# Optimization experiments

Measured on AMD Instinct MI355X. Metric: run time of the kernel, lower is better.

Reference implementation:

```python
import jax, jax.numpy as jnp
import numpy as np

N, E, F, H = 50000, 1_600_000, 6, 64


def setup_inputs() -> dict:
    key = jax.random.key(0)
    ks = jax.random.split(key, 12)
    inp = {
        "vertex_features": jax.random.normal(ks[0], (N, F), dtype=jnp.float32),
        "edges": jax.random.randint(ks[1], (2, E), 0, N, dtype=jnp.int64 if jax.config.jax_enable_x64 else jnp.int32),
        "weights": jax.random.uniform(ks[2], (E,), dtype=jnp.float32),
        # GCNConv layer params (glorot-ish scale) + biases (PyG default bias=True)
        "W1": jax.random.normal(ks[3], (F, H), dtype=jnp.float32) / np.sqrt(F),
        "b1": jnp.zeros((H,), jnp.float32),
        "W2": jax.random.normal(ks[4], (H, H), dtype=jnp.float32) / np.sqrt(H),
        "b2": jnp.zeros((H,), jnp.float32),
        "W3": jax.random.normal(ks[5], (H, H), dtype=jnp.float32) / np.sqrt(H),
        "b3": jnp.zeros((H,), jnp.float32),
        "Wl": jax.random.normal(ks[6], (H, 1), dtype=jnp.float32) / np.sqrt(H),
        "bl": jnp.zeros((1,), jnp.float32),
    }
    return inp


def _gcn_norm(edges, weights, n):
    # PyG gcn_norm: add self loops (weight 1), symmetric D^-1/2 A D^-1/2;
    # degree computed at target nodes (edge_index[1], flow source_to_target).
    row, col = edges[0], edges[1]
    loop = jnp.arange(n, dtype=row.dtype)
    row_f = jnp.concatenate([row, loop])
    col_f = jnp.concatenate([col, loop])
    w_f = jnp.concatenate([weights, jnp.ones((n,), weights.dtype)])
    deg = jax.ops.segment_sum(w_f, col_f, num_segments=n)
    dis = jnp.where(deg > 0, jax.lax.rsqrt(jnp.maximum(deg, 1e-30)), 0.0)
    norm = dis[row_f] * w_f * dis[col_f]
    return row_f, col_f, norm


def _gcn_conv(x, W, b, row, col, norm, n):
    xw = x @ W                                   # [n, H_out]
    agg = jax.ops.segment_sum(norm[:, None] * xw[row], col, num_segments=n)
    return agg + b


def reference(vertex_features, edges, weights, W1, b1, W2, b2, W3, b3, Wl, bl):
    n = vertex_features.shape[0]
    row, col, norm = _gcn_norm(edges, weights, n)  # norm identical for all layers
    h = jax.nn.sigmoid(_gcn_conv(vertex_features, W1, b1, row, col, norm, n))
    h = jax.nn.sigmoid(_gcn_conv(h, W2, b2, row, col, norm, n))
    h = jax.nn.sigmoid(_gcn_conv(h, W3, b3, row, col, norm, n))
    logits = h @ Wl + bl                           # [n, 1]
    return jax.nn.softmax(logits, axis=0)          # softmax over node dim
```

## Files before the change

### kernel.cpp

```cpp
#include <hip/hip_runtime.h>
#include <math.h>


#define BLK 256
#define SKB 256
#define CHUNK 4096

typedef __attribute__((ext_vector_type(8))) short bf16x8;
typedef __attribute__((ext_vector_type(4))) float f32x4;

__device__ inline unsigned short f2bf(float f) {
  unsigned u = __float_as_uint(f);
  return (unsigned short)((u + 0x7FFF + ((u >> 16) & 1)) >> 16);
}
__device__ inline float bflo(unsigned u) { return __uint_as_float(u << 16); }
__device__ inline float bfhi(unsigned u) { return __uint_as_float(u & 0xFFFF0000u); }


__global__ __launch_bounds__(256) void k_binscatter(
    const int* __restrict__ row, const int* __restrict__ col,
    const float* __restrict__ w, int E,
    int* __restrict__ bfill, int2* __restrict__ bucket, int CAP) {
  __shared__ int2 stage[CHUNK];
  __shared__ int lhist[SKB], lbase[SKB], gbase[SKB], lfill[SKB];
  int t = threadIdx.x;
  int e0 = blockIdx.x * CHUNK;
  int n = E - e0; if (n > CHUNK) n = CHUNK;
  lhist[t] = 0; lfill[t] = 0;
  __syncthreads();
  for (int i = t; i < n; i += BLK) atomicAdd(&lhist[((unsigned)col[e0 + i]) >> 8], 1);
  __syncthreads();
  lbase[t] = lhist[t];
  __syncthreads();
  for (int off = 1; off < SKB; off <<= 1) {
    int v = (t >= off) ? lbase[t - off] : 0;
    __syncthreads();
    lbase[t] += v;
    __syncthreads();
  }
  int excl = lbase[t] - lhist[t];
  int cb = lhist[t];
  gbase[t] = cb ? atomicAdd(&bfill[t << 4], cb) : 0;
  __syncthreads();
  lbase[t] = excl;
  __syncthreads();
  for (int i = t; i < n; i += BLK) {
    int c = col[e0 + i];
    int b = ((unsigned)c) >> 8;
    int r = atomicAdd(&lfill[b], 1);
    stage[lbase[b] + r] = make_int2(row[e0 + i] | (c << 16), __float_as_int(w[e0 + i]));
  }
  __syncthreads();
  for (int i = t; i < n; i += BLK) {
    int2 p = stage[i];
    int b = ((unsigned)p.x) >> 24;
    bucket[(size_t)b * CAP + gbase[b] + (i - lbase[b])] = p;
  }
}


__global__ __launch_bounds__(256) void k_build(
    const int2* __restrict__ bucket, const int* __restrict__ bfill,
    const float* __restrict__ x,
    unsigned* __restrict__ csr, int* __restrict__ cnt, int* __restrict__ start,
    float* __restrict__ dis, unsigned short* __restrict__ x8b, int CAP, int N) {
  __shared__ int   hist[SKB];
  __shared__ float wsum[SKB];
  __shared__ int   lstart[SKB + 1];
  __shared__ int   lfill[SKB];
  int b = blockIdx.x, t = threadIdx.x;
  int n0 = b << 8;
  int M = N - n0; if (M > 256) M = 256;
  if (M <= 0) return;
  hist[t] = 0; wsum[t] = 0.0f; lfill[t] = 0;
  __syncthreads();
  const int2* bb = bucket + (size_t)b * CAP;
  int ec = bfill[b << 4];
  for (int i = t; i < ec; i += BLK) {
    int2 p = bb[i];
    int lc = (((unsigned)p.x) >> 16) & 255;
    atomicAdd(&hist[lc], 1);
    atomicAdd(&wsum[lc], __int_as_float(p.y));
  }
  __syncthreads();
  if (t == 0) {
    int run = 0;
    for (int i = 0; i < M; ++i) { lstart[i] = run; run += hist[i]; }
    lstart[M] = run;
  }
  __syncthreads();
  if (t < M) {
    int n = n0 + t;
    cnt[n] = hist[t];
    start[n] = b * CAP + lstart[t];
    float d = 1.0f / sqrtf(wsum[t] + 1.0f);
    dis[n] = d;
    const float* xr = x + (size_t)n * 6;
    uint4 pk;
    pk.x = (unsigned)f2bf(d * xr[0]) | ((unsigned)f2bf(d * xr[1]) << 16);
    pk.y = (unsigned)f2bf(d * xr[2]) | ((unsigned)f2bf(d * xr[3]) << 16);
    pk.z = (unsigned)f2bf(d * xr[4]) | ((unsigned)f2bf(d * xr[5]) << 16);
    pk.w = 0u;
    *(uint4*)(x8b + (size_t)n * 8) = pk;
  }
  __syncthreads();
  for (int i = t; i < ec; i += BLK) {
    int2 p = bb[i];
    int lc = (((unsigned)p.x) >> 16) & 255;
    int pos = lstart[lc] + atomicAdd(&lfill[lc], 1);
    csr[(size_t)b * CAP + pos] =
        ((unsigned)p.x & 0xFFFFu) | ((unsigned)f2bf(__int_as_float(p.y)) << 16);
  }
}


__global__ void k_wprep(const float* __restrict__ W2, const float* __restrict__ W3,
                        unsigned short* __restrict__ W2b, unsigned short* __restrict__ W3b) {
  int i = blockIdx.x * blockDim.x + threadIdx.x;
  if (i < 4096) { W2b[i] = f2bf(W2[i]); W3b[i] = f2bf(W3[i]); }
}


__global__ void k_layer1(const unsigned short* __restrict__ x8b,
                         const int* __restrict__ start, const int* __restrict__ cnt,
                         const unsigned* __restrict__ csr, const float* __restrict__ dis,
                         const float* __restrict__ W1, const float* __restrict__ b1,
                         unsigned short* __restrict__ hb, int N) {
  int n = blockIdx.x * blockDim.x + threadIdx.x;
  if (n >= N) return;
  uint4 sv = *(const uint4*)(x8b + (size_t)n * 8);
  float a0 = bflo(sv.x), a1 = bfhi(sv.x), a2 = bflo(sv.y);
  float a3 = bfhi(sv.y), a4 = bflo(sv.z), a5 = bfhi(sv.z);
  int s = start[n], e = s + cnt[n];
  int i = s;
  for (; i + 4 <= e; i += 4) {
    unsigned p0 = csr[i], p1 = csr[i + 1], p2 = csr[i + 2], p3 = csr[i + 3];
    uint4 h0 = *(const uint4*)(x8b + (size_t)(p0 & 0xFFFFu) * 8);
    uint4 h1 = *(const uint4*)(x8b + (size_t)(p1 & 0xFFFFu) * 8);
    uint4 h2 = *(const uint4*)(x8b + (size_t)(p2 & 0xFFFFu) * 8);
    uint4 h3 = *(const uint4*)(x8b + (size_t)(p3 & 0xFFFFu) * 8);
    float v0 = bfhi(p0), v1 = bfhi(p1), v2 = bfhi(p2), v3 = bfhi(p3);
    a0 += v0*bflo(h0.x) + v1*bflo(h1.x) + v2*bflo(h2.x) + v3*bflo(h3.x);
    a1 += v0*bfhi(h0.x) + v1*bfhi(h1.x) + v2*bfhi(h2.x) + v3*bfhi(h3.x);
    a2 += v0*bflo(h0.y) + v1*bflo(h1.y) + v2*bflo(h2.y) + v3*bflo(h3.y);
    a3 += v0*bfhi(h0.y) + v1*bfhi(h1.y) + v2*bfhi(h2.y) + v3*bfhi(h3.y);
    a4 += v0*bflo(h0.z) + v1*bflo(h1.z) + v2*bflo(h2.z) + v3*bflo(h3.z);
    a5 += v0*bfhi(h0.z) + v1*bfhi(h1.z) + v2*bfhi(h2.z) + v3*bfhi(h3.z);
  }
  for (; i < e; ++i) {
    unsigned pe = csr[i];
    float v = bfhi(pe);
    uint4 hv = *(const uint4*)(x8b + (size_t)(pe & 0xFFFFu) * 8);
    a0 += v * bflo(hv.x); a1 += v * bfhi(hv.x);
    a2 += v * bflo(hv.y); a3 += v * bfhi(hv.y);
    a4 += v * bflo(hv.z); a5 += v * bfhi(hv.z);
  }
  float d = dis[n];
  a0 *= d; a1 *= d; a2 *= d; a3 *= d; a4 *= d; a5 *= d;
  unsigned short* o = hb + (size_t)n * 64;
#pragma unroll
  for (int j4 = 0; j4 < 16; ++j4) {
    float4 acc = *(const float4*)(b1 + j4 * 4);
    const float* Wc = W1 + j4 * 4;
    acc.x += a0*Wc[0] + a1*Wc[64] + a2*Wc[128] + a3*Wc[192] + a4*Wc[256] + a5*Wc[320];
    acc.y += a0*Wc[1] + a1*Wc[65] + a2*Wc[129] + a3*Wc[193] + a4*Wc[257] + a5*Wc[321];
    acc.z += a0*Wc[2] + a1*Wc[66] + a2*Wc[130] + a3*Wc[194] + a4*Wc[258] + a5*Wc[322];
    acc.w += a0*Wc[3] + a1*Wc[67] + a2*Wc[131] + a3*Wc[195] + a4*Wc[259] + a5*Wc[323];
    uint2 pk;
    pk.x = (unsigned)f2bf(d / (1.0f + expf(-acc.x))) |
           ((unsigned)f2bf(d / (1.0f + expf(-acc.y))) << 16);
    pk.y = (unsigned)f2bf(d / (1.0f + expf(-acc.z))) |
           ((unsigned)f2bf(d / (1.0f + expf(-acc.w))) << 16);
    *(uint2*)(o + j4 * 4) = pk;
  }
}


__global__ void k_agg64(const unsigned short* __restrict__ hb,
                        const int* __restrict__ start, const int* __restrict__ cnt,
                        const unsigned* __restrict__ csr, const float* __restrict__ dis,
                        unsigned short* __restrict__ aggb, int N) {
  int t = blockIdx.x * blockDim.x + threadIdx.x;
  int n = t >> 3, sub = t & 7;
  if (n >= N) return;
  uint4 sv = *(const uint4*)(hb + (size_t)n * 64 + sub * 8);
  float a0 = bflo(sv.x), a1 = bfhi(sv.x), a2 = bflo(sv.y), a3 = bfhi(sv.y);
  float a4 = bflo(sv.z), a5 = bfhi(sv.z), a6 = bflo(sv.w), a7 = bfhi(sv.w);
  int s = start[n], e = s + cnt[n];
  int i = s;
  for (; i + 4 <= e; i += 4) {
    unsigned p0 = csr[i], p1 = csr[i + 1], p2 = csr[i + 2], p3 = csr[i + 3];
    uint4 h0 = *(const uint4*)(hb + (size_t)(p0 & 0xFFFFu) * 64 + sub * 8);
    uint4 h1 = *(const uint4*)(hb + (size_t)(p1 & 0xFFFFu) * 64 + sub * 8);
    uint4 h2 = *(const uint4*)(hb + (size_t)(p2 & 0xFFFFu) * 64 + sub * 8);
    uint4 h3 = *(const uint4*)(hb + (size_t)(p3 & 0xFFFFu) * 64 + sub * 8);
    float v0 = bfhi(p0), v1 = bfhi(p1), v2 = bfhi(p2), v3 = bfhi(p3);
    a0 += v0*bflo(h0.x) + v1*bflo(h1.x) + v2*bflo(h2.x) + v3*bflo(h3.x);
    a1 += v0*bfhi(h0.x) + v1*bfhi(h1.x) + v2*bfhi(h2.x) + v3*bfhi(h3.x);
    a2 += v0*bflo(h0.y) + v1*bflo(h1.y) + v2*bflo(h2.y) + v3*bflo(h3.y);
    a3 += v0*bfhi(h0.y) + v1*bfhi(h1.y) + v2*bfhi(h2.y) + v3*bfhi(h3.y);
    a4 += v0*bflo(h0.z) + v1*bflo(h1.z) + v2*bflo(h2.z) + v3*bflo(h3.z);
    a5 += v0*bfhi(h0.z) + v1*bfhi(h1.z) + v2*bfhi(h2.z) + v3*bfhi(h3.z);
    a6 += v0*bflo(h0.w) + v1*bflo(h1.w) + v2*bflo(h2.w) + v3*bflo(h3.w);
    a7 += v0*bfhi(h0.w) + v1*bfhi(h1.w) + v2*bfhi(h2.w) + v3*bfhi(h3.w);
  }
  for (; i < e; ++i) {
    unsigned pe = csr[i];
    float v = bfhi(pe);
    uint4 hv = *(const uint4*)(hb + (size_t)(pe & 0xFFFFu) * 64 + sub * 8);
    a0 += v * bflo(hv.x); a1 += v * bfhi(hv.x);
    a2 += v * bflo(hv.y); a3 += v * bfhi(hv.y);
    a4 += v * bflo(hv.z); a5 += v * bfhi(hv.z);
    a6 += v * bflo(hv.w); a7 += v * bfhi(hv.w);
  }
  float d = dis[n];
  uint4 pk;
  pk.x = (unsigned)f2bf(d * a0) | ((unsigned)f2bf(d * a1) << 16);
  pk.y = (unsigned)f2bf(d * a2) | ((unsigned)f2bf(d * a3) << 16);
  pk.z = (unsigned)f2bf(d * a4) | ((unsigned)f2bf(d * a5) << 16);
  pk.w = (unsigned)f2bf(d * a6) | ((unsigned)f2bf(d * a7) << 16);
  *(uint4*)(aggb + (size_t)n * 64 + sub * 8) = pk;
}


__global__ __launch_bounds__(256) void k_dense64_mfma(
    const unsigned short* __restrict__ aggb, const unsigned short* __restrict__ Wb,
    const float* __restrict__ b, const float* __restrict__ dis,
    unsigned short* __restrict__ hb, int NS) {
  int wid = threadIdx.x >> 6, lane = threadIdx.x & 63;
  int quad = lane >> 4, r16 = lane & 15;
  bf16x8 Bf[2][4];
#pragma unroll
  for (int kt = 0; kt < 2; ++kt)
#pragma unroll
    for (int jt = 0; jt < 4; ++jt)
#pragma unroll
      for (int j = 0; j < 8; ++j)
        Bf[kt][jt][j] = (short)Wb[(kt * 32 + quad * 8 + j) * 64 + jt * 16 + r16];
  float bias[4];
#pragma unroll
  for (int jt = 0; jt < 4; ++jt) bias[jt] = b[jt * 16 + r16];
  int stride = gridDim.x * 4;
  for (int s = blockIdx.x * 4 + wid; s < NS; s += stride) {
    int n0 = s * 16;
    bf16x8 Af0 = *(const bf16x8*)(aggb + (size_t)(n0 + r16) * 64 + quad * 8);
    bf16x8 Af1 = *(const bf16x8*)(aggb + (size_t)(n0 + r16) * 64 + 32 + quad * 8);
    f32x4 C[4];
#pragma unroll
    for (int jt = 0; jt < 4; ++jt) {
      f32x4 z = {0.f, 0.f, 0.f, 0.f};
      z = __builtin_amdgcn_mfma_f32_16x16x32_bf16(Af0, Bf[0][jt], z, 0, 0, 0);
      z = __builtin_amdgcn_mfma_f32_16x16x32_bf16(Af1, Bf[1][jt], z, 0, 0, 0);
      C[jt] = z;
    }
    float dv[4];
#pragma unroll
    for (int reg = 0; reg < 4; ++reg) dv[reg] = dis[n0 + quad * 4 + reg];
#pragma unroll
    for (int jt = 0; jt < 4; ++jt)
#pragma unroll
      for (int reg = 0; reg < 4; ++reg) {
        float h = dv[reg] / (1.0f + expf(-(C[jt][reg] + bias[jt])));
        hb[(size_t)(n0 + quad * 4 + reg) * 64 + jt * 16 + r16] = f2bf(h);
      }
  }
}


__global__ __launch_bounds__(256) void k_head_mfma(
    const unsigned short* __restrict__ aggb, const unsigned short* __restrict__ Wb,
    const float* __restrict__ b, const float* __restrict__ Wl,
    const float* __restrict__ bl, float* __restrict__ expv,
    float* __restrict__ red_part, int NS) {
  int wid = threadIdx.x >> 6, lane = threadIdx.x & 63;
  int quad = lane >> 4, r16 = lane & 15;
  bf16x8 Bf[2][4];
#pragma unroll
  for (int kt = 0; kt < 2; ++kt)
#pragma unroll
    for (int jt = 0; jt < 4; ++jt)
#pragma unroll
      for (int j = 0; j < 8; ++j)
        Bf[kt][jt][j] = (short)Wb[(kt * 32 + quad * 8 + j) * 64 + jt * 16 + r16];
  float bias[4], wlv[4];
#pragma unroll
  for (int jt = 0; jt < 4; ++jt) {
    bias[jt] = b[jt * 16 + r16];
    wlv[jt]  = Wl[jt * 16 + r16];
  }
  float bl0 = bl[0];
  float lsum = 0.0f;
  int stride = gridDim.x * 4;
  for (int s = blockIdx.x * 4 + wid; s < NS; s += stride) {
    int n0 = s * 16;
    bf16x8 Af0 = *(const bf16x8*)(aggb + (size_t)(n0 + r16) * 64 + quad * 8);
    bf16x8 Af1 = *(const bf16x8*)(aggb + (size_t)(n0 + r16) * 64 + 32 + quad * 8);
    f32x4 C[4];
#pragma unroll
    for (int jt = 0; jt < 4; ++jt) {
      f32x4 z = {0.f, 0.f, 0.f, 0.f};
      z = __builtin_amdgcn_mfma_f32_16x16x32_bf16(Af0, Bf[0][jt], z, 0, 0, 0);
      z = __builtin_amdgcn_mfma_f32_16x16x32_bf16(Af1, Bf[1][jt], z, 0, 0, 0);
      C[jt] = z;
    }
    float p0 = 0, p1 = 0, p2 = 0, p3 = 0;
#pragma unroll
    for (int jt = 0; jt < 4; ++jt) {
      p0 += wlv[jt] / (1.0f + expf(-(C[jt][0] + bias[jt])));
      p1 += wlv[jt] / (1.0f + expf(-(C[jt][1] + bias[jt])));
      p2 += wlv[jt] / (1.0f + expf(-(C[jt][2] + bias[jt])));
      p3 += wlv[jt] / (1.0f + expf(-(C[jt][3] + bias[jt])));
    }
#pragma unroll
    for (int m = 1; m < 16; m <<= 1) {
      p0 += __shfl_xor(p0, m, 64);
      p1 += __shfl_xor(p1, m, 64);
      p2 += __shfl_xor(p2, m, 64);
      p3 += __shfl_xor(p3, m, 64);
    }
    float ls = 0.0f;
    if (r16 == 0) {
      float e0 = expf(p0 + bl0), e1 = expf(p1 + bl0);
      float e2 = expf(p2 + bl0), e3 = expf(p3 + bl0);
      int r = n0 + quad * 4;
      expv[r] = e0; expv[r + 1] = e1; expv[r + 2] = e2; expv[r + 3] = e3;
      ls = e0 + e1 + e2 + e3;
    }
    ls += __shfl_xor(ls, 16, 64);
    ls += __shfl_xor(ls, 32, 64);
    lsum += ls;
  }
  if (lane == 0) atomicAdd(&red_part[(blockIdx.x & 63) << 4], lsum);
}

__global__ void k_out(const float* __restrict__ expv, int N,
                      const float* __restrict__ red_part, float* __restrict__ out) {
  int i = blockIdx.x * blockDim.x + threadIdx.x;
  int lane = threadIdx.x & 63;
  float s = red_part[lane << 4];
#pragma unroll
  for (int o = 32; o > 0; o >>= 1) s += __shfl_down(s, o, 64);
  s = __shfl(s, 0, 64);
  if (i < N) out[i] = expv[i] / s;
}


extern "C" void kernel_launch(void* const* d_in, const int* in_sizes, int n_in,
                              void* d_out, int out_size, void* d_ws, size_t ws_size,
                              hipStream_t stream) {
  const float* x   = (const float*)d_in[0];
  const int*   edg = (const int*)d_in[1];
  const float* w   = (const float*)d_in[2];
  const float* W1  = (const float*)d_in[3];
  const float* b1  = (const float*)d_in[4];
  const float* W2  = (const float*)d_in[5];
  const float* b2  = (const float*)d_in[6];
  const float* W3  = (const float*)d_in[7];
  const float* b3  = (const float*)d_in[8];
  const float* Wl  = (const float*)d_in[9];
  const float* bl  = (const float*)d_in[10];
  float* out = (float*)d_out;

  const int N = in_sizes[0] / 6;
  const int E = in_sizes[2];
  const int* row = edg;
  const int* col = edg + E;
  const int NB = (N + 255) >> 8;
  const int NS = (N + 15) / 16;

  size_t off = 0;
  char* base = (char*)d_ws;
  auto alloc = [&](size_t bytes) -> void* {
    void* p = base + off;
    off += (bytes + 255) & ~(size_t)255;
    return p;
  };
  int*   bfill    = (int*)alloc((size_t)SKB * 16 * 4);
  float* red_part = (float*)alloc((size_t)64 * 16 * 4);
  size_t zero_bytes = off;
  int*   cnt    = (int*)alloc((size_t)N * 4);
  int*   start  = (int*)alloc((size_t)N * 4);
  float* dis    = (float*)alloc((size_t)N * 4);
  float* expv   = (float*)alloc((size_t)N * 4);
  unsigned short* x8b = (unsigned short*)alloc((size_t)N * 8 * 2);
  unsigned short* hb  = (unsigned short*)alloc((size_t)N * 64 * 2);
  unsigned short* W2b = (unsigned short*)alloc(4096 * 2);
  unsigned short* W3b = (unsigned short*)alloc(4096 * 2);
  size_t remain = (ws_size > off) ? (ws_size - off) : 0;
  long long capn = ((long long)remain) / ((long long)NB * 12);
  int CAP = (int)capn;
  if (CAP > 9216) CAP = 9216;
  if (CAP < 8704) CAP = 8704;
  unsigned* csr = (unsigned*)alloc((size_t)NB * CAP * 4);
  size_t aggsz = (size_t)N * 64 * 2;
  size_t bksz  = (size_t)NB * CAP * 8;
  void* shared_blk = alloc(aggsz > bksz ? aggsz : bksz);
  int2*           bucket = (int2*)shared_blk;
  unsigned short* aggb   = (unsigned short*)shared_blk;

  const int gE  = (E + CHUNK - 1) / CHUNK;
  const int gN  = (N + BLK - 1) / BLK;
  const int gN8 = (N * 8 + BLK - 1) / BLK;
  const int gM  = 200;

  hipMemsetAsync(d_ws, 0, zero_bytes, stream);

  k_wprep     <<<16, BLK, 0, stream>>>(W2, W3, W2b, W3b);
  k_binscatter<<<gE, BLK, 0, stream>>>(row, col, w, E, bfill, bucket, CAP);
  k_build     <<<NB, BLK, 0, stream>>>(bucket, bfill, x, csr, cnt, start, dis, x8b, CAP, N);

  k_layer1<<<gN, BLK, 0, stream>>>(x8b, start, cnt, csr, dis, W1, b1, hb, N);

  k_agg64       <<<gN8, BLK, 0, stream>>>(hb, start, cnt, csr, dis, aggb, N);
  k_dense64_mfma<<<gM,  BLK, 0, stream>>>(aggb, W2b, b2, dis, hb, NS);

  k_agg64    <<<gN8, BLK, 0, stream>>>(hb, start, cnt, csr, dis, aggb, N);
  k_head_mfma<<<gM,  BLK, 0, stream>>>(aggb, W3b, b3, Wl, bl, expv, red_part, NS);

  k_out<<<gN, BLK, 0, stream>>>(expv, N, red_part, out);
}
```

Measured before the change: 232.4 us.

## Unroll gathers by eight, widen build blocks, fold weight prep into build

The CSR gather loops in layer1 and agg64 go from 4-way to 8-way unrolled, so more independent neighbor loads are in flight per thread. k_build now runs with 512 threads per block and gains 8 extra blocks that do the bf16 conversion of W2/W3, which removes the separate k_wprep launch. The binscatter CHUNK is halved, giving more, smaller scatter blocks. The wider unroll raises register pressure, and the mix of unrelated tweaks can pull in different directions.

```diff
diff --git a/kernel.cpp b/kernel.cpp
--- a/kernel.cpp
+++ b/kernel.cpp
@@ -3,8 +3,9 @@
 
 
 #define BLK 256
+#define BLKB 512
 #define SKB 256
-#define CHUNK 4096
+#define CHUNK 2048
 
 typedef __attribute__((ext_vector_type(8))) short bf16x8;
 typedef __attribute__((ext_vector_type(4))) float f32x4;
@@ -59,24 +60,31 @@
 }
 
 
-__global__ __launch_bounds__(256) void k_build(
+__global__ __launch_bounds__(512) void k_build(
     const int2* __restrict__ bucket, const int* __restrict__ bfill,
     const float* __restrict__ x,
     unsigned* __restrict__ csr, int* __restrict__ cnt, int* __restrict__ start,
-    float* __restrict__ dis, unsigned short* __restrict__ x8b, int CAP, int N) {
+    float* __restrict__ dis, unsigned short* __restrict__ x8b, int CAP, int N,
+    int NBb, const float* __restrict__ W2, const float* __restrict__ W3,
+    unsigned short* __restrict__ W2b, unsigned short* __restrict__ W3b) {
   __shared__ int   hist[SKB];
   __shared__ float wsum[SKB];
   __shared__ int   lstart[SKB + 1];
   __shared__ int   lfill[SKB];
   int b = blockIdx.x, t = threadIdx.x;
+  if (b >= NBb) {
+    int i = (b - NBb) * BLKB + t;
+    if (i < 4096) { W2b[i] = f2bf(W2[i]); W3b[i] = f2bf(W3[i]); }
+    return;
+  }
   int n0 = b << 8;
   int M = N - n0; if (M > 256) M = 256;
   if (M <= 0) return;
-  hist[t] = 0; wsum[t] = 0.0f; lfill[t] = 0;
+  if (t < SKB) { hist[t] = 0; wsum[t] = 0.0f; lfill[t] = 0; }
   __syncthreads();
   const int2* bb = bucket + (size_t)b * CAP;
   int ec = bfill[b << 4];
-  for (int i = t; i < ec; i += BLK) {
+  for (int i = t; i < ec; i += BLKB) {
     int2 p = bb[i];
     int lc = (((unsigned)p.x) >> 16) & 255;
     atomicAdd(&hist[lc], 1);
@@ -104,20 +112,13 @@
     *(uint4*)(x8b + (size_t)n * 8) = pk;
   }
   __syncthreads();
-  for (int i = t; i < ec; i += BLK) {
+  for (int i = t; i < ec; i += BLKB) {
     int2 p = bb[i];
     int lc = (((unsigned)p.x) >> 16) & 255;
     int pos = lstart[lc] + atomicAdd(&lfill[lc], 1);
     csr[(size_t)b * CAP + pos] =
         ((unsigned)p.x & 0xFFFFu) | ((unsigned)f2bf(__int_as_float(p.y)) << 16);
   }
-}
-
-
-__global__ void k_wprep(const float* __restrict__ W2, const float* __restrict__ W3,
-                        unsigned short* __restrict__ W2b, unsigned short* __restrict__ W3b) {
-  int i = blockIdx.x * blockDim.x + threadIdx.x;
-  if (i < 4096) { W2b[i] = f2bf(W2[i]); W3b[i] = f2bf(W3[i]); }
 }
 
 
@@ -133,19 +134,31 @@
   float a3 = bfhi(sv.y), a4 = bflo(sv.z), a5 = bfhi(sv.z);
   int s = start[n], e = s + cnt[n];
   int i = s;
-  for (; i + 4 <= e; i += 4) {
-    unsigned p0 = csr[i], p1 = csr[i + 1], p2 = csr[i + 2], p3 = csr[i + 3];
+  for (; i + 8 <= e; i += 8) {
+    unsigned p0 = csr[i],     p1 = csr[i + 1], p2 = csr[i + 2], p3 = csr[i + 3];
+    unsigned p4 = csr[i + 4], p5 = csr[i + 5], p6 = csr[i + 6], p7 = csr[i + 7];
     uint4 h0 = *(const uint4*)(x8b + (size_t)(p0 & 0xFFFFu) * 8);
     uint4 h1 = *(const uint4*)(x8b + (size_t)(p1 & 0xFFFFu) * 8);
     uint4 h2 = *(const uint4*)(x8b + (size_t)(p2 & 0xFFFFu) * 8);
     uint4 h3 = *(const uint4*)(x8b + (size_t)(p3 & 0xFFFFu) * 8);
+    uint4 h4 = *(const uint4*)(x8b + (size_t)(p4 & 0xFFFFu) * 8);
+    uint4 h5 = *(const uint4*)(x8b + (size_t)(p5 & 0xFFFFu) * 8);
+    uint4 h6 = *(const uint4*)(x8b + (size_t)(p6 & 0xFFFFu) * 8);
+    uint4 h7 = *(const uint4*)(x8b + (size_t)(p7 & 0xFFFFu) * 8);
     float v0 = bfhi(p0), v1 = bfhi(p1), v2 = bfhi(p2), v3 = bfhi(p3);
-    a0 += v0*bflo(h0.x) + v1*bflo(h1.x) + v2*bflo(h2.x) + v3*bflo(h3.x);
-    a1 += v0*bfhi(h0.x) + v1*bfhi(h1.x) + v2*bfhi(h2.x) + v3*bfhi(h3.x);
-    a2 += v0*bflo(h0.y) + v1*bflo(h1.y) + v2*bflo(h2.y) + v3*bflo(h3.y);
-    a3 += v0*bfhi(h0.y) + v1*bfhi(h1.y) + v2*bfhi(h2.y) + v3*bfhi(h3.y);
-    a4 += v0*bflo(h0.z) + v1*bflo(h1.z) + v2*bflo(h2.z) + v3*bflo(h3.z);
-    a5 += v0*bfhi(h0.z) + v1*bfhi(h1.z) + v2*bfhi(h2.z) + v3*bfhi(h3.z);
+    float v4 = bfhi(p4), v5 = bfhi(p5), v6 = bfhi(p6), v7 = bfhi(p7);
+    a0 += v0*bflo(h0.x) + v1*bflo(h1.x) + v2*bflo(h2.x) + v3*bflo(h3.x)
+        + v4*bflo(h4.x) + v5*bflo(h5.x) + v6*bflo(h6.x) + v7*bflo(h7.x);
+    a1 += v0*bfhi(h0.x) + v1*bfhi(h1.x) + v2*bfhi(h2.x) + v3*bfhi(h3.x)
+        + v4*bfhi(h4.x) + v5*bfhi(h5.x) + v6*bfhi(h6.x) + v7*bfhi(h7.x);
+    a2 += v0*bflo(h0.y) + v1*bflo(h1.y) + v2*bflo(h2.y) + v3*bflo(h3.y)
+        + v4*bflo(h4.y) + v5*bflo(h5.y) + v6*bflo(h6.y) + v7*bflo(h7.y);
+    a3 += v0*bfhi(h0.y) + v1*bfhi(h1.y) + v2*bfhi(h2.y) + v3*bfhi(h3.y)
+        + v4*bfhi(h4.y) + v5*bfhi(h5.y) + v6*bfhi(h6.y) + v7*bfhi(h7.y);
+    a4 += v0*bflo(h0.z) + v1*bflo(h1.z) + v2*bflo(h2.z) + v3*bflo(h3.z)
+        + v4*bflo(h4.z) + v5*bflo(h5.z) + v6*bflo(h6.z) + v7*bflo(h7.z);
+    a5 += v0*bfhi(h0.z) + v1*bfhi(h1.z) + v2*bfhi(h2.z) + v3*bfhi(h3.z)
+        + v4*bfhi(h4.z) + v5*bfhi(h5.z) + v6*bfhi(h6.z) + v7*bfhi(h7.z);
   }
   for (; i < e; ++i) {
     unsigned pe = csr[i];
@@ -188,21 +201,35 @@
   float a4 = bflo(sv.z), a5 = bfhi(sv.z), a6 = bflo(sv.w), a7 = bfhi(sv.w);
   int s = start[n], e = s + cnt[n];
   int i = s;
-  for (; i + 4 <= e; i += 4) {
-    unsigned p0 = csr[i], p1 = csr[i + 1], p2 = csr[i + 2], p3 = csr[i + 3];
+  for (; i + 8 <= e; i += 8) {
+    unsigned p0 = csr[i],     p1 = csr[i + 1], p2 = csr[i + 2], p3 = csr[i + 3];
+    unsigned p4 = csr[i + 4], p5 = csr[i + 5], p6 = csr[i + 6], p7 = csr[i + 7];
     uint4 h0 = *(const uint4*)(hb + (size_t)(p0 & 0xFFFFu) * 64 + sub * 8);
     uint4 h1 = *(const uint4*)(hb + (size_t)(p1 & 0xFFFFu) * 64 + sub * 8);
     uint4 h2 = *(const uint4*)(hb + (size_t)(p2 & 0xFFFFu) * 64 + sub * 8);
     uint4 h3 = *(const uint4*)(hb + (size_t)(p3 & 0xFFFFu) * 64 + sub * 8);
+    uint4 h4 = *(const uint4*)(hb + (size_t)(p4 & 0xFFFFu) * 64 + sub * 8);
+    uint4 h5 = *(const uint4*)(hb + (size_t)(p5 & 0xFFFFu) * 64 + sub * 8);
+    uint4 h6 = *(const uint4*)(hb + (size_t)(p6 & 0xFFFFu) * 64 + sub * 8);
+    uint4 h7 = *(const uint4*)(hb + (size_t)(p7 & 0xFFFFu) * 64 + sub * 8);
     float v0 = bfhi(p0), v1 = bfhi(p1), v2 = bfhi(p2), v3 = bfhi(p3);
-    a0 += v0*bflo(h0.x) + v1*bflo(h1.x) + v2*bflo(h2.x) + v3*bflo(h3.x);
-    a1 += v0*bfhi(h0.x) + v1*bfhi(h1.x) + v2*bfhi(h2.x) + v3*bfhi(h3.x);
-    a2 += v0*bflo(h0.y) + v1*bflo(h1.y) + v2*bflo(h2.y) + v3*bflo(h3.y);
-    a3 += v0*bfhi(h0.y) + v1*bfhi(h1.y) + v2*bfhi(h2.y) + v3*bfhi(h3.y);
-    a4 += v0*bflo(h0.z) + v1*bflo(h1.z) + v2*bflo(h2.z) + v3*bflo(h3.z);
-    a5 += v0*bfhi(h0.z) + v1*bfhi(h1.z) + v2*bfhi(h2.z) + v3*bfhi(h3.z);
-    a6 += v0*bflo(h0.w) + v1*bflo(h1.w) + v2*bflo(h2.w) + v3*bflo(h3.w);
-    a7 += v0*bfhi(h0.w) + v1*bfhi(h1.w) + v2*bfhi(h2.w) + v3*bfhi(h3.w);
+    float v4 = bfhi(p4), v5 = bfhi(p5), v6 = bfhi(p6), v7 = bfhi(p7);
+    a0 += v0*bflo(h0.x) + v1*bflo(h1.x) + v2*bflo(h2.x) + v3*bflo(h3.x)
+        + v4*bflo(h4.x) + v5*bflo(h5.x) + v6*bflo(h6.x) + v7*bflo(h7.x);
+    a1 += v0*bfhi(h0.x) + v1*bfhi(h1.x) + v2*bfhi(h2.x) + v3*bfhi(h3.x)
+        + v4*bfhi(h4.x) + v5*bfhi(h5.x) + v6*bfhi(h6.x) + v7*bfhi(h7.x);
+    a2 += v0*bflo(h0.y) + v1*bflo(h1.y) + v2*bflo(h2.y) + v3*bflo(h3.y)
+        + v4*bflo(h4.y) + v5*bflo(h5.y) + v6*bflo(h6.y) + v7*bflo(h7.y);
+    a3 += v0*bfhi(h0.y) + v1*bfhi(h1.y) + v2*bfhi(h2.y) + v3*bfhi(h3.y)
+        + v4*bfhi(h4.y) + v5*bfhi(h5.y) + v6*bfhi(h6.y) + v7*bfhi(h7.y);
+    a4 += v0*bflo(h0.z) + v1*bflo(h1.z) + v2*bflo(h2.z) + v3*bflo(h3.z)
+        + v4*bflo(h4.z) + v5*bflo(h5.z) + v6*bflo(h6.z) + v7*bflo(h7.z);
+    a5 += v0*bfhi(h0.z) + v1*bfhi(h1.z) + v2*bfhi(h2.z) + v3*bfhi(h3.z)
+        + v4*bfhi(h4.z) + v5*bfhi(h5.z) + v6*bfhi(h6.z) + v7*bfhi(h7.z);
+    a6 += v0*bflo(h0.w) + v1*bflo(h1.w) + v2*bflo(h2.w) + v3*bflo(h3.w)
+        + v4*bflo(h4.w) + v5*bflo(h5.w) + v6*bflo(h6.w) + v7*bflo(h7.w);
+    a7 += v0*bfhi(h0.w) + v1*bfhi(h1.w) + v2*bfhi(h2.w) + v3*bfhi(h3.w)
+        + v4*bfhi(h4.w) + v5*bfhi(h5.w) + v6*bfhi(h6.w) + v7*bfhi(h7.w);
   }
   for (; i < e; ++i) {
     unsigned pe = csr[i];
@@ -402,12 +429,13 @@
   const int gN  = (N + BLK - 1) / BLK;
   const int gN8 = (N * 8 + BLK - 1) / BLK;
   const int gM  = 200;
+  const int gB  = NB + 8;
 
   hipMemsetAsync(d_ws, 0, zero_bytes, stream);
 
-  k_wprep     <<<16, BLK, 0, stream>>>(W2, W3, W2b, W3b);
   k_binscatter<<<gE, BLK, 0, stream>>>(row, col, w, E, bfill, bucket, CAP);
-  k_build     <<<NB, BLK, 0, stream>>>(bucket, bfill, x, csr, cnt, start, dis, x8b, CAP, N);
+  k_build     <<<gB, BLKB, 0, stream>>>(bucket, bfill, x, csr, cnt, start, dis,
+                                        x8b, CAP, N, NB, W2, W3, W2b, W3b);
 
   k_layer1<<<gN, BLK, 0, stream>>>(x8b, start, cnt, csr, dis, W1, b1, hb, N);
 
```

Measured after the change: 238.9 us. 1.03x slower.
